# Kernel optimization log

Hardware: AMD Instinct MI355X
Metric: run time of the kernel (lower is better)

## Reference

```python
import jax, jax.numpy as jnp
import numpy as np

N, E, D, H = 50000, 640000, 128, 8
d = D // H  # per-head dim


def layernorm(x, g, b, eps=1e-5):
    mu = jnp.mean(x, axis=-1, keepdims=True)
    var = jnp.var(x, axis=-1, keepdims=True)
    return (x - mu) * jax.lax.rsqrt(var + eps) * g + b


def setup_inputs() -> dict:
    key = jax.random.key(0)
    ks = jax.random.split(key, 14)
    s = 0.05
    return {
        "node_emb": jax.random.normal(ks[0], (N, D), jnp.float32),
        "bond_emb": jax.random.normal(ks[1], (E, D), jnp.float32),
        "basic_attn": jax.random.uniform(ks[2], (E,), jnp.float32),
        "src": jax.random.randint(ks[3], (E,), 0, N),
        "dst": jax.random.randint(ks[4], (E,), 0, N),
        "Wk": jax.random.normal(ks[5], (D, D), jnp.float32) * s,
        "Wq": jax.random.normal(ks[6], (D, D), jnp.float32) * s,
        "Wv": jax.random.normal(ks[7], (D, D), jnp.float32) * s,
        "W_dis": jax.random.normal(ks[8], (1, H), jnp.float32) * s,
        "W_beta": jax.random.normal(ks[9], (3 * D, 1), jnp.float32) * s,
        "ln1_g": jnp.ones((D,), jnp.float32),
        "ln1_b": jnp.zeros((D,), jnp.float32),
        "W_ff1": jax.random.normal(ks[10], (D, 2 * D), jnp.float32) * s,
        "W_ff2": jax.random.normal(ks[11], (2 * D, D), jnp.float32) * s,
    }


def reference(node_emb, bond_emb, basic_attn, src, dst, Wk, Wq, Wv, W_dis,
              W_beta, ln1_g, ln1_b, W_ff1, W_ff2):
    n = node_emb.shape[0]
    # Q/K/V projections (eval mode: dropouts are identity)
    k = (node_emb @ Wk).reshape(n, H, d)
    q = (node_emb @ Wq).reshape(n, H, d)
    v = (bond_emb @ Wv).reshape(-1, H, d)          # per-edge values [E,H,d]
    # per-edge dot-product score (fn.u_dot_v) scaled by sqrt(out_feat)
    scores = jnp.einsum('ehd,ehd->eh', k[src], q[dst])
    scores = scores / jnp.sqrt(jnp.asarray(d, scores.dtype))
    # learned distance decay: Linear(1,H) on basic_attn
    dist = basic_attn[:, None] @ W_dis             # [E,H]
    logits = scores + dist
    # edge_softmax over in-edges of each destination node, per head
    mx = jax.ops.segment_max(logits, dst, num_segments=n)
    mx = jnp.where(jnp.isfinite(mx), mx, 0.0)
    e = jnp.exp(logits - mx[dst])
    den = jax.ops.segment_sum(e, dst, num_segments=n)
    att = e / (den[dst] + 1e-16)                   # [E,H]
    # message = v * att, scatter-sum to destination nodes
    ft = jax.ops.segment_sum(v * att[:, :, None], dst, num_segments=n)
    he = ft.reshape(n, D)
    # beta gating
    beta = jax.nn.sigmoid(
        jnp.concatenate([he, node_emb, he - node_emb], axis=-1) @ W_beta)
    he = beta * node_emb + (1.0 - beta) * he
    # FFN with pre-LN and identity-initialized post-LN
    h = layernorm(he, ln1_g, ln1_b)
    out = jax.nn.relu(h @ W_ff1) @ W_ff2
    ones = jnp.ones((D,), he.dtype)
    zeros = jnp.zeros((D,), he.dtype)
    return layernorm(out + he, ones, zeros)
```

## Files before the change

### kernel.cpp

```cpp
#include <hip/hip_runtime.h>
#include <math.h>

#define NN 50000
#define NE 640000
#define DIM 128
#define NH 8

typedef unsigned short u16;
typedef __attribute__((ext_vector_type(8))) short short8;
typedef __attribute__((ext_vector_type(4))) float f32x4;

__device__ __forceinline__ float wave_sum64(float v) {
  #pragma unroll
  for (int m = 32; m >= 1; m >>= 1) v += __shfl_xor(v, m, 64);
  return v;
}
__device__ __forceinline__ unsigned bf16pk(float a, float b) {
  unsigned ua = __float_as_uint(a); ua = (ua + 0x7fffu + ((ua >> 16) & 1u)) >> 16;
  unsigned ub = __float_as_uint(b); ub = (ub + 0x7fffu + ((ub >> 16) & 1u)) & 0xffff0000u;
  return ua | ub;
}
__device__ __forceinline__ u16 bf16c(float x) {
  unsigned u = __float_as_uint(x);
  return (u16)((u + 0x7fffu + ((u >> 16) & 1u)) >> 16);
}
__device__ __forceinline__ float bf_lo(unsigned v) { return __uint_as_float(v << 16); }
__device__ __forceinline__ float bf_hi(unsigned v) { return __uint_as_float(v & 0xffff0000u); }

#define AS1(p) ((const __attribute__((address_space(1))) unsigned*)(p))
#define AS3(p) ((__attribute__((address_space(3))) unsigned*)(p))

__global__ __launch_bounds__(256) void prep_k(
    const float* __restrict__ node, unsigned* __restrict__ node16,
    const float* __restrict__ Wq, const float* __restrict__ Wk,
    const float* __restrict__ W1, const float* __restrict__ W2,
    u16* __restrict__ Wtq, u16* __restrict__ Wtk,
    u16* __restrict__ Wt1, u16* __restrict__ Wt2,
    const int* __restrict__ dst, int* __restrict__ deg) {
  int b = blockIdx.x, tid = threadIdx.x;
  if (b < 12500) {
    int t = b * 256 + tid;
    float2 v = *(const float2*)(node + (size_t)2 * t);
    node16[t] = bf16pk(v.x, v.y);
  } else if (b < 12564) {
    int t = (b - 12500) * 256 + tid;
    int n = t >> 7, k = t & 127;
    Wtq[t] = bf16c(Wq[(size_t)k * 128 + n]);
  } else if (b < 12628) {
    int t = (b - 12564) * 256 + tid;
    int n = t >> 7, k = t & 127;
    Wtk[t] = bf16c(Wk[(size_t)k * 128 + n]);
  } else if (b < 12756) {
    int t = (b - 12628) * 256 + tid;
    int n = t >> 7, k = t & 127;
    Wt1[t] = bf16c(W1[(size_t)k * 256 + n]);
  } else if (b < 12884) {
    int t = (b - 12756) * 256 + tid;
    int n = t >> 8, k = t & 255;
    Wt2[t] = bf16c(W2[(size_t)k * 128 + n]);
  } else {
    int e = (b - 12884) * 256 + tid;
    atomicAdd(&deg[dst[e]], 1);
  }
}

#define SCAN_T 1024
#define SCHUNK 49
__global__ __launch_bounds__(1024) void scan_k(const int* __restrict__ deg,
                                               int* __restrict__ off,
                                               int* __restrict__ cursor) {
  __shared__ int part[SCAN_T];
  int t = threadIdx.x;
  int lo = t * SCHUNK, hi = lo + SCHUNK; if (hi > NN) hi = NN;
  int s = 0;
  for (int i = lo; i < hi; ++i) s += deg[i];
  part[t] = s;
  __syncthreads();
  for (int o = 1; o < SCAN_T; o <<= 1) {
    int v = (t >= o) ? part[t - o] : 0;
    __syncthreads();
    part[t] += v;
    __syncthreads();
  }
  int base = (t == 0) ? 0 : part[t - 1];
  for (int i = lo; i < hi; ++i) {
    off[i] = base; cursor[i] = base; base += deg[i];
  }
  if (t == SCAN_T - 1) off[NN] = part[SCAN_T - 1];
}

__global__ __launch_bounds__(256) void csr_fill_k(const int* __restrict__ dst,
                                                  int* __restrict__ cursor,
                                                  int* __restrict__ eids) {
  int e = blockIdx.x * 256 + threadIdx.x;
  if (e < NE) {
    int p = atomicAdd(&cursor[dst[e]], 1);
    eids[p] = e;
  }
}

__global__ __launch_bounds__(256) void qk_mfma_k(
    const u16* __restrict__ A, const u16* __restrict__ Wtq,
    const u16* __restrict__ Wtk, u16* __restrict__ qo,
    u16* __restrict__ ko) {
  __shared__ u16 At[64 * 128];
  const int wid = threadIdx.x >> 6, l = threadIdx.x & 63;
  const int quad = l >> 4, l16 = l & 15;
  const int c0 = (wid & 1) * 64;
  const u16* wt = (wid < 2) ? Wtq : Wtk;
  u16* ob = (wid < 2) ? qo : ko;
  short8 bfr[4][4];
  #pragma unroll
  for (int ct = 0; ct < 4; ++ct)
    #pragma unroll
    for (int ks = 0; ks < 4; ++ks)
      bfr[ct][ks] = *(const short8*)(wt + (c0 + ct * 16 + l16) * 128 + ks * 32 + quad * 8);
  const int ntiles = (NN + 63) / 64;
  for (int t = blockIdx.x; t < ntiles; t += gridDim.x) {
    const char* gsrc = (const char*)A + (size_t)t * 64 * 128 * 2;
    #pragma unroll
    for (int i = 0; i < 4; ++i) {
      int dbase = wid * 4096 + i * 1024;
      int soff = (dbase + l * 16) ^ ((((i * 4) + (l >> 4)) & 7) << 4);
      __builtin_amdgcn_global_load_lds(AS1(gsrc + soff),
                                       AS3((char*)At + dbase), 16, 0, 0);
    }
    __syncthreads();
    f32x4 acc[4][4];
    #pragma unroll
    for (int rt = 0; rt < 4; ++rt)
      #pragma unroll
      for (int ct = 0; ct < 4; ++ct)
        acc[rt][ct] = (f32x4){0.f, 0.f, 0.f, 0.f};
    #pragma unroll
    for (int ks = 0; ks < 4; ++ks) {
      short8 af[4];
      #pragma unroll
      for (int rt = 0; rt < 4; ++rt) {
        int bo = (((rt * 16 + l16) * 128 + ks * 32 + quad * 8) * 2) ^ ((l16 & 7) << 4);
        af[rt] = *(const short8*)((const char*)At + bo);
      }
      #pragma unroll
      for (int rt = 0; rt < 4; ++rt)
        #pragma unroll
        for (int ct = 0; ct < 4; ++ct)
          acc[rt][ct] = __builtin_amdgcn_mfma_f32_16x16x32_bf16(
              af[rt], bfr[ct][ks], acc[rt][ct], 0, 0, 0);
    }
    __syncthreads();
    #pragma unroll
    for (int rt = 0; rt < 4; ++rt)
      #pragma unroll
      for (int r = 0; r < 4; ++r) {
        int row = t * 64 + rt * 16 + quad * 4 + r;
        if (row < NN) {
          u16* op = ob + (size_t)row * 128 + c0 + l16;
          #pragma unroll
          for (int ct = 0; ct < 4; ++ct) op[ct * 16] = bf16c(acc[rt][ct][r]);
        }
      }
  }
}

__global__ __launch_bounds__(256) void ffn_mfma_k(
    const u16* __restrict__ A, const u16* __restrict__ Wt1,
    const u16* __restrict__ Wt2, const float* __restrict__ he,
    float* __restrict__ outp) {
  __shared__ __align__(16) u16 At[64 * 128];
  __shared__ __align__(16) u16 Ht[64 * 256];
  __shared__ float redS[4][64], redQ[4][64];
  const int wid = threadIdx.x >> 6, l = threadIdx.x & 63;
  const int quad = l >> 4, l16 = l & 15;
  const int c1 = wid * 64;
  const int c2 = wid * 32;
  const int ntiles = (NN + 63) / 64;
  for (int t = blockIdx.x; t < ntiles; t += gridDim.x) {
    short8 b1f[4][4];
    #pragma unroll
    for (int ct = 0; ct < 4; ++ct)
      #pragma unroll
      for (int ks = 0; ks < 4; ++ks)
        b1f[ct][ks] = *(const short8*)(Wt1 + (c1 + ct * 16 + l16) * 128 + ks * 32 + quad * 8);
    const char* gsrc = (const char*)A + (size_t)t * 64 * 128 * 2;
    #pragma unroll
    for (int i = 0; i < 4; ++i) {
      int dbase = wid * 4096 + i * 1024;
      int soff = (dbase + l * 16) ^ ((((i * 4) + (l >> 4)) & 7) << 4);
      __builtin_amdgcn_global_load_lds(AS1(gsrc + soff),
                                       AS3((char*)At + dbase), 16, 0, 0);
    }
    __syncthreads();
    f32x4 acc1[4][4];
    #pragma unroll
    for (int rt = 0; rt < 4; ++rt)
      #pragma unroll
      for (int ct = 0; ct < 4; ++ct)
        acc1[rt][ct] = (f32x4){0.f, 0.f, 0.f, 0.f};
    #pragma unroll
    for (int ks = 0; ks < 4; ++ks) {
      short8 af[4];
      #pragma unroll
      for (int rt = 0; rt < 4; ++rt) {
        int bo = (((rt * 16 + l16) * 128 + ks * 32 + quad * 8) * 2) ^ ((l16 & 7) << 4);
        af[rt] = *(const short8*)((const char*)At + bo);
      }
      #pragma unroll
      for (int rt = 0; rt < 4; ++rt)
        #pragma unroll
        for (int ct = 0; ct < 4; ++ct)
          acc1[rt][ct] = __builtin_amdgcn_mfma_f32_16x16x32_bf16(
              af[rt], b1f[ct][ks], acc1[rt][ct], 0, 0, 0);
    }
    #pragma unroll
    for (int rt = 0; rt < 4; ++rt)
      #pragma unroll
      for (int r = 0; r < 4; ++r) {
        int row = rt * 16 + quad * 4 + r;
        #pragma unroll
        for (int ct = 0; ct < 4; ++ct) {
          int col = c1 + ct * 16 + l16;
          int bo = (row * 512 + col * 2) ^ ((row & 7) << 4);
          *(u16*)((char*)Ht + bo) = bf16c(fmaxf(acc1[rt][ct][r], 0.f));
        }
      }
    __syncthreads();
    short8 b2f[2][8];
    #pragma unroll
    for (int ct = 0; ct < 2; ++ct)
      #pragma unroll
      for (int ks = 0; ks < 8; ++ks)
        b2f[ct][ks] = *(const short8*)(Wt2 + (c2 + ct * 16 + l16) * 256 + ks * 32 + quad * 8);
    f32x4 acc2[4][2];
    #pragma unroll
    for (int rt = 0; rt < 4; ++rt)
      #pragma unroll
      for (int ct = 0; ct < 2; ++ct)
        acc2[rt][ct] = (f32x4){0.f, 0.f, 0.f, 0.f};
    #pragma unroll
    for (int ks = 0; ks < 8; ++ks) {
      short8 af[4];
      #pragma unroll
      for (int rt = 0; rt < 4; ++rt) {
        int bo = ((rt * 16 + l16) * 512 + ks * 64 + quad * 16) ^ ((l16 & 7) << 4);
        af[rt] = *(const short8*)((const char*)Ht + bo);
      }
      #pragma unroll
      for (int rt = 0; rt < 4; ++rt)
        #pragma unroll
        for (int ct = 0; ct < 2; ++ct)
          acc2[rt][ct] = __builtin_amdgcn_mfma_f32_16x16x32_bf16(
              af[rt], b2f[ct][ks], acc2[rt][ct], 0, 0, 0);
    }
    #pragma unroll
    for (int rt = 0; rt < 4; ++rt)
      #pragma unroll
      for (int r = 0; r < 4; ++r) {
        int row = rt * 16 + quad * 4 + r;
        int grow = t * 64 + row;
        float h0 = 0.f, h1 = 0.f;
        if (grow < NN) {
          h0 = he[(size_t)grow * 128 + c2 + l16];
          h1 = he[(size_t)grow * 128 + c2 + 16 + l16];
        }
        float z0 = acc2[rt][0][r] + h0;
        float z1 = acc2[rt][1][r] + h1;
        acc2[rt][0][r] = z0; acc2[rt][1][r] = z1;
        float ps = z0 + z1;
        float pq = fmaf(z0, z0, z1 * z1);
        ps += __shfl_xor(ps, 1, 64);  pq += __shfl_xor(pq, 1, 64);
        ps += __shfl_xor(ps, 2, 64);  pq += __shfl_xor(pq, 2, 64);
        ps += __shfl_xor(ps, 4, 64);  pq += __shfl_xor(pq, 4, 64);
        ps += __shfl_xor(ps, 8, 64);  pq += __shfl_xor(pq, 8, 64);
        if (l16 == 0) { redS[wid][row] = ps; redQ[wid][row] = pq; }
      }
    __syncthreads();
    #pragma unroll
    for (int rt = 0; rt < 4; ++rt)
      #pragma unroll
      for (int r = 0; r < 4; ++r) {
        int row = rt * 16 + quad * 4 + r;
        int grow = t * 64 + row;
        float s4 = redS[0][row] + redS[1][row] + redS[2][row] + redS[3][row];
        float q4 = redQ[0][row] + redQ[1][row] + redQ[2][row] + redQ[3][row];
        float mu = s4 * (1.f / 128.f);
        float vr = q4 * (1.f / 128.f) - mu * mu;
        float rs = rsqrtf(vr + 1e-5f);
        if (grow < NN) {
          outp[(size_t)grow * 128 + c2 + l16]      = (acc2[rt][0][r] - mu) * rs;
          outp[(size_t)grow * 128 + c2 + 16 + l16] = (acc2[rt][1][r] - mu) * rs;
        }
      }
  }
}

__global__ __launch_bounds__(256) void edge_exp_k(
    const unsigned* __restrict__ kb16, const unsigned* __restrict__ qb16,
    const float* __restrict__ ba, const int* __restrict__ src,
    const int* __restrict__ dst, const float* __restrict__ Wdis,
    const int* __restrict__ eids, float* __restrict__ exs) {
  int idx = blockIdx.x * 256 + threadIdx.x;
  if (idx >= NE * NH) return;
  int p = idx >> 3, h = idx & 7;
  int e = eids[p];
  int s = src[e], t = dst[e];
  const uint4* kp = (const uint4*)(kb16 + (size_t)s * 64 + h * 8);
  const uint4* qp = (const uint4*)(qb16 + (size_t)t * 64 + h * 8);
  uint4 A0 = kp[0], A1 = kp[1];
  uint4 B0 = qp[0], B1 = qp[1];
  float sc = 0.f;
  sc = fmaf(bf_lo(A0.x), bf_lo(B0.x), sc); sc = fmaf(bf_hi(A0.x), bf_hi(B0.x), sc);
  sc = fmaf(bf_lo(A0.y), bf_lo(B0.y), sc); sc = fmaf(bf_hi(A0.y), bf_hi(B0.y), sc);
  sc = fmaf(bf_lo(A0.z), bf_lo(B0.z), sc); sc = fmaf(bf_hi(A0.z), bf_hi(B0.z), sc);
  sc = fmaf(bf_lo(A0.w), bf_lo(B0.w), sc); sc = fmaf(bf_hi(A0.w), bf_hi(B0.w), sc);
  sc = fmaf(bf_lo(A1.x), bf_lo(B1.x), sc); sc = fmaf(bf_hi(A1.x), bf_hi(B1.x), sc);
  sc = fmaf(bf_lo(A1.y), bf_lo(B1.y), sc); sc = fmaf(bf_hi(A1.y), bf_hi(B1.y), sc);
  sc = fmaf(bf_lo(A1.z), bf_lo(B1.z), sc); sc = fmaf(bf_hi(A1.z), bf_hi(B1.z), sc);
  sc = fmaf(bf_lo(A1.w), bf_lo(B1.w), sc); sc = fmaf(bf_hi(A1.w), bf_hi(B1.w), sc);
  exs[idx] = __expf(sc * 0.25f + ba[e] * Wdis[h]);
}

__global__ __launch_bounds__(512, 6) void node_attn_k(
    const float* __restrict__ bond, const float* __restrict__ WvG,
    const float* __restrict__ exs, const int* __restrict__ off,
    const int* __restrict__ eids, const float* __restrict__ x,
    const float* __restrict__ Wb, const float* __restrict__ g1,
    const float* __restrict__ b1, float* __restrict__ he,
    unsigned* __restrict__ hbuf16) {
  __shared__ unsigned Wvpk[DIM * 64];
  __shared__ unsigned gbuf[8][NH][67];
  for (int t = threadIdx.x; t < DIM * 64; t += 512) {
    int i = t >> 6, c = t & 63;
    Wvpk[t] = bf16pk(WvG[i * DIM + c], WvG[i * DIM + c + 64]);
  }
  __syncthreads();
  const int wid = threadIdx.x >> 6, l = threadIdx.x & 63;
  const int hh = l & 7;
  const float wb0 = Wb[l],         wb1 = Wb[l + 64];
  const float wb2 = Wb[DIM + l],   wb3 = Wb[DIM + l + 64];
  const float wb4 = Wb[2*DIM + l], wb5 = Wb[2*DIM + l + 64];
  const float gl0 = g1[l], gl1 = g1[l + 64];
  const float bl0 = b1[l], bl1 = b1[l + 64];

  for (int n = blockIdx.x * 8 + wid; n < NN; n += gridDim.x * 8) {
    int o0 = __builtin_amdgcn_readfirstlane(off[n]);
    int o1 = __builtin_amdgcn_readfirstlane(off[n + 1]);
    int deg = o1 - o0;
    float acc[16];
    #pragma unroll
    for (int i = 0; i < 16; ++i) acc[i] = 0.f;
    float d0 = 0.f, d1 = 0.f, d2 = 0.f, d3 = 0.f;
    float d4 = 0.f, d5 = 0.f, d6 = 0.f, d7 = 0.f;

    for (int g = 0; g < deg; g += 8) {
      float2 bc[8];
      #pragma unroll
      for (int s = 0; s < 8; ++s) {
        if (g + s < deg) {
          int e = eids[o0 + g + s];
          bc[s] = *(const float2*)(bond + (size_t)e * DIM + 2 * l);
        }
      }
      #pragma unroll
      for (int s = 0; s < 8; ++s) {
        if (g + s < deg) {
          const float4* ep = (const float4*)(exs) + (size_t)(o0 + g + s) * 2;
          float4 ea = ep[0], eb = ep[1];
          d0 += ea.x; d1 += ea.y; d2 += ea.z; d3 += ea.w;
          d4 += eb.x; d5 += eb.y; d6 += eb.z; d7 += eb.w;
          float2 bv = bc[s];
          acc[0]  = fmaf(ea.x, bv.x, acc[0]);  acc[1]  = fmaf(ea.x, bv.y, acc[1]);
          acc[2]  = fmaf(ea.y, bv.x, acc[2]);  acc[3]  = fmaf(ea.y, bv.y, acc[3]);
          acc[4]  = fmaf(ea.z, bv.x, acc[4]);  acc[5]  = fmaf(ea.z, bv.y, acc[5]);
          acc[6]  = fmaf(ea.w, bv.x, acc[6]);  acc[7]  = fmaf(ea.w, bv.y, acc[7]);
          acc[8]  = fmaf(eb.x, bv.x, acc[8]);  acc[9]  = fmaf(eb.x, bv.y, acc[9]);
          acc[10] = fmaf(eb.y, bv.x, acc[10]); acc[11] = fmaf(eb.y, bv.y, acc[11]);
          acc[12] = fmaf(eb.z, bv.x, acc[12]); acc[13] = fmaf(eb.z, bv.y, acc[13]);
          acc[14] = fmaf(eb.w, bv.x, acc[14]); acc[15] = fmaf(eb.w, bv.y, acc[15]);
        }
      }
    }
    float dsa = (hh & 1) ? d1 : d0, dsb = (hh & 1) ? d3 : d2;
    float dsc = (hh & 1) ? d5 : d4, dsd = (hh & 1) ? d7 : d6;
    float dse = (hh & 2) ? dsb : dsa, dsf = (hh & 2) ? dsd : dsc;
    float dsel = (hh & 4) ? dsf : dse;
    float rden = 1.f / (dsel + 1e-16f);
    #pragma unroll
    for (int h = 0; h < 8; ++h) {
      float rh = __shfl(rden, h, 64);
      acc[2 * h] *= rh; acc[2 * h + 1] *= rh;
    }
    #pragma unroll
    for (int h = 0; h < 8; ++h)
      gbuf[wid][h][l] = bf16pk(acc[2 * h], acc[2 * h + 1]);
    int h0 = l >> 4, h1 = 4 + (l >> 4);
    float f0 = 0.f, f1 = 0.f;
    #pragma unroll 8
    for (int ii = 0; ii < 64; ++ii) {
      unsigned u = gbuf[wid][h0][ii];
      unsigned v = gbuf[wid][h1][ii];
      unsigned w0 = Wvpk[(2 * ii) * 64 + l];
      unsigned w1 = Wvpk[(2 * ii + 1) * 64 + l];
      f0 = fmaf(bf_lo(u), bf_lo(w0), f0); f0 = fmaf(bf_hi(u), bf_lo(w1), f0);
      f1 = fmaf(bf_lo(v), bf_hi(w0), f1); f1 = fmaf(bf_hi(v), bf_hi(w1), f1);
    }
    float x0 = x[(size_t)n * DIM + l], x1 = x[(size_t)n * DIM + l + 64];
    float s = f0 * wb0 + x0 * wb2 + (f0 - x0) * wb4
            + f1 * wb1 + x1 * wb3 + (f1 - x1) * wb5;
    s = wave_sum64(s);
    float beta = 1.f / (1.f + __expf(-s));
    float he0 = beta * x0 + (1.f - beta) * f0;
    float he1 = beta * x1 + (1.f - beta) * f1;
    he[(size_t)n * DIM + l] = he0;
    he[(size_t)n * DIM + l + 64] = he1;
    float mu = wave_sum64(he0 + he1) * (1.f / DIM);
    float vr = wave_sum64(he0 * he0 + he1 * he1) * (1.f / DIM) - mu * mu;
    float rs = rsqrtf(vr + 1e-5f);
    float v0 = (he0 - mu) * rs * gl0 + bl0;
    float v1 = (he1 - mu) * rs * gl1 + bl1;
    int i0 = (2 * l) & 63, i1 = (2 * l + 1) & 63;
    float a0 = __shfl(v0, i0, 64), b0 = __shfl(v1, i0, 64);
    float a1 = __shfl(v0, i1, 64), b1v = __shfl(v1, i1, 64);
    float c0 = (l < 32) ? a0 : b0;
    float c1 = (l < 32) ? a1 : b1v;
    hbuf16[(size_t)n * 64 + l] = bf16pk(c0, c1);
  }
}

extern "C" void kernel_launch(void* const* d_in, const int* in_sizes, int n_in,
                              void* d_out, int out_size, void* d_ws, size_t ws_size,
                              hipStream_t stream) {
  const float* node = (const float*)d_in[0];
  const float* bond = (const float*)d_in[1];
  const float* ba   = (const float*)d_in[2];
  const int*   src  = (const int*)  d_in[3];
  const int*   dst  = (const int*)  d_in[4];
  const float* Wk   = (const float*)d_in[5];
  const float* Wq   = (const float*)d_in[6];
  const float* Wv   = (const float*)d_in[7];
  const float* Wdis = (const float*)d_in[8];
  const float* Wb   = (const float*)d_in[9];
  const float* g1   = (const float*)d_in[10];
  const float* b1   = (const float*)d_in[11];
  const float* W1   = (const float*)d_in[12];
  const float* W2   = (const float*)d_in[13];
  float* out = (float*)d_out;

  char* W = (char*)d_ws;
  u16* node16 = (u16*)(W);
  u16* qb16   = (u16*)(W + 13000000);
  u16* kb16   = (u16*)(W + 26000000);
  u16* hbuf16 = (u16*)(W + 26000000);
  float* exs  = (float*)(W + 39000000);
  float* he   = (float*)(W + 64600000);
  u16* Wtq    = (u16*)(W + 90200000);
  u16* Wtk    = Wtq + 128 * 128;
  u16* Wt1    = Wtk + 128 * 128;
  u16* Wt2    = Wt1 + 256 * 128;
  int* deg    = (int*)(W + 90400000);
  int* off    = deg + (NN + 1);
  int* cursor = off + (NN + 1);
  int* eids   = cursor + (NN + 1);

  hipMemsetAsync(deg, 0, (size_t)(NN + 1) * 4, stream);

  prep_k<<<15384, 256, 0, stream>>>(node, (unsigned*)node16, Wq, Wk, W1, W2,
                                    Wtq, Wtk, Wt1, Wt2, dst, deg);
  scan_k<<<1, 1024, 0, stream>>>(deg, off, cursor);
  csr_fill_k<<<(NE + 255) / 256, 256, 0, stream>>>(dst, cursor, eids);

  const int ntiles = (NN + 63) / 64;

  qk_mfma_k<<<ntiles, 256, 0, stream>>>(node16, Wtq, Wtk, qb16, kb16);

  edge_exp_k<<<(NE * NH + 255) / 256, 256, 0, stream>>>(
      (const unsigned*)kb16, (const unsigned*)qb16, ba, src, dst, Wdis, eids, exs);

  node_attn_k<<<3125, 512, 0, stream>>>(bond, Wv, exs, off, eids, node,
                                        Wb, g1, b1, he, (unsigned*)hbuf16);

  ffn_mfma_k<<<ntiles, 256, 0, stream>>>(hbuf16, Wt1, Wt2, he, out);
}
```

Before: 858.6 us.

## Fuse edge score and exp computation into node attention kernel

Removes the separate edge_exp_k kernel and computes the per-edge q·k dot product, distance bias and exp inside node_attn_k. Each lane loads one packed bf16 pair of k for the source node, reduces over the 8 lanes of a head with xor shuffles, and broadcasts the per-head exp values across the wave. This drops the exs buffer write and read and one kernel launch, in exchange for extra shuffles and a dependent src gather inside the aggregation loop. The gbuf row is also padded to 68 words and read as 16-byte vectors in the Wv projection loop.

```diff
diff --git a/kernel.cpp b/kernel.cpp
--- a/kernel.cpp
+++ b/kernel.cpp
@@ -293,48 +293,24 @@
   }
 }
 
-__global__ __launch_bounds__(256) void edge_exp_k(
-    const unsigned* __restrict__ kb16, const unsigned* __restrict__ qb16,
-    const float* __restrict__ ba, const int* __restrict__ src,
-    const int* __restrict__ dst, const float* __restrict__ Wdis,
-    const int* __restrict__ eids, float* __restrict__ exs) {
-  int idx = blockIdx.x * 256 + threadIdx.x;
-  if (idx >= NE * NH) return;
-  int p = idx >> 3, h = idx & 7;
-  int e = eids[p];
-  int s = src[e], t = dst[e];
-  const uint4* kp = (const uint4*)(kb16 + (size_t)s * 64 + h * 8);
-  const uint4* qp = (const uint4*)(qb16 + (size_t)t * 64 + h * 8);
-  uint4 A0 = kp[0], A1 = kp[1];
-  uint4 B0 = qp[0], B1 = qp[1];
-  float sc = 0.f;
-  sc = fmaf(bf_lo(A0.x), bf_lo(B0.x), sc); sc = fmaf(bf_hi(A0.x), bf_hi(B0.x), sc);
-  sc = fmaf(bf_lo(A0.y), bf_lo(B0.y), sc); sc = fmaf(bf_hi(A0.y), bf_hi(B0.y), sc);
-  sc = fmaf(bf_lo(A0.z), bf_lo(B0.z), sc); sc = fmaf(bf_hi(A0.z), bf_hi(B0.z), sc);
-  sc = fmaf(bf_lo(A0.w), bf_lo(B0.w), sc); sc = fmaf(bf_hi(A0.w), bf_hi(B0.w), sc);
-  sc = fmaf(bf_lo(A1.x), bf_lo(B1.x), sc); sc = fmaf(bf_hi(A1.x), bf_hi(B1.x), sc);
-  sc = fmaf(bf_lo(A1.y), bf_lo(B1.y), sc); sc = fmaf(bf_hi(A1.y), bf_hi(B1.y), sc);
-  sc = fmaf(bf_lo(A1.z), bf_lo(B1.z), sc); sc = fmaf(bf_hi(A1.z), bf_hi(B1.z), sc);
-  sc = fmaf(bf_lo(A1.w), bf_lo(B1.w), sc); sc = fmaf(bf_hi(A1.w), bf_hi(B1.w), sc);
-  exs[idx] = __expf(sc * 0.25f + ba[e] * Wdis[h]);
-}
-
 __global__ __launch_bounds__(512, 6) void node_attn_k(
     const float* __restrict__ bond, const float* __restrict__ WvG,
-    const float* __restrict__ exs, const int* __restrict__ off,
-    const int* __restrict__ eids, const float* __restrict__ x,
+    const unsigned* __restrict__ qb16, const unsigned* __restrict__ kb16,
+    const float* __restrict__ ba, const int* __restrict__ srcv,
+    const int* __restrict__ off, const int* __restrict__ eids,
+    const float* __restrict__ x, const float* __restrict__ Wdis,
     const float* __restrict__ Wb, const float* __restrict__ g1,
     const float* __restrict__ b1, float* __restrict__ he,
     unsigned* __restrict__ hbuf16) {
   __shared__ unsigned Wvpk[DIM * 64];
-  __shared__ unsigned gbuf[8][NH][67];
+  __shared__ __align__(16) unsigned gbuf[8][NH][68];
   for (int t = threadIdx.x; t < DIM * 64; t += 512) {
     int i = t >> 6, c = t & 63;
     Wvpk[t] = bf16pk(WvG[i * DIM + c], WvG[i * DIM + c + 64]);
   }
   __syncthreads();
   const int wid = threadIdx.x >> 6, l = threadIdx.x & 63;
-  const int hh = l & 7;
+  const float wdis_l = Wdis[l >> 3];
   const float wb0 = Wb[l],         wb1 = Wb[l + 64];
   const float wb2 = Wb[DIM + l],   wb3 = Wb[DIM + l + 64];
   const float wb4 = Wb[2*DIM + l], wb5 = Wb[2*DIM + l + 64];
@@ -345,63 +321,76 @@
     int o0 = __builtin_amdgcn_readfirstlane(off[n]);
     int o1 = __builtin_amdgcn_readfirstlane(off[n + 1]);
     int deg = o1 - o0;
+    unsigned ql = qb16[(size_t)n * 64 + l];
+    float qlo = bf_lo(ql), qhi = bf_hi(ql);
     float acc[16];
     #pragma unroll
     for (int i = 0; i < 16; ++i) acc[i] = 0.f;
-    float d0 = 0.f, d1 = 0.f, d2 = 0.f, d3 = 0.f;
-    float d4 = 0.f, d5 = 0.f, d6 = 0.f, d7 = 0.f;
+    float dsum = 0.f;
 
     for (int g = 0; g < deg; g += 8) {
-      float2 bc[8];
+      int eg[8]; unsigned kc[8]; float2 bc[8];
       #pragma unroll
       for (int s = 0; s < 8; ++s) {
         if (g + s < deg) {
           int e = eids[o0 + g + s];
+          eg[s] = e;
+          kc[s] = kb16[(size_t)srcv[e] * 64 + l];
           bc[s] = *(const float2*)(bond + (size_t)e * DIM + 2 * l);
         }
       }
       #pragma unroll
       for (int s = 0; s < 8; ++s) {
         if (g + s < deg) {
-          const float4* ep = (const float4*)(exs) + (size_t)(o0 + g + s) * 2;
-          float4 ea = ep[0], eb = ep[1];
-          d0 += ea.x; d1 += ea.y; d2 += ea.z; d3 += ea.w;
-          d4 += eb.x; d5 += eb.y; d6 += eb.z; d7 += eb.w;
+          float p = bf_lo(kc[s]) * qlo;
+          p = fmaf(bf_hi(kc[s]), qhi, p);
+          p += __shfl_xor(p, 1, 64);
+          p += __shfl_xor(p, 2, 64);
+          p += __shfl_xor(p, 4, 64);
+          float ex = __expf(fmaf(ba[eg[s]], wdis_l, p * 0.25f));
+          dsum += ex;
+          float a0 = __shfl(ex, 0, 64),  a1 = __shfl(ex, 8, 64);
+          float a2 = __shfl(ex, 16, 64), a3 = __shfl(ex, 24, 64);
+          float a4 = __shfl(ex, 32, 64), a5 = __shfl(ex, 40, 64);
+          float a6 = __shfl(ex, 48, 64), a7 = __shfl(ex, 56, 64);
           float2 bv = bc[s];
-          acc[0]  = fmaf(ea.x, bv.x, acc[0]);  acc[1]  = fmaf(ea.x, bv.y, acc[1]);
-          acc[2]  = fmaf(ea.y, bv.x, acc[2]);  acc[3]  = fmaf(ea.y, bv.y, acc[3]);
-          acc[4]  = fmaf(ea.z, bv.x, acc[4]);  acc[5]  = fmaf(ea.z, bv.y, acc[5]);
-          acc[6]  = fmaf(ea.w, bv.x, acc[6]);  acc[7]  = fmaf(ea.w, bv.y, acc[7]);
-          acc[8]  = fmaf(eb.x, bv.x, acc[8]);  acc[9]  = fmaf(eb.x, bv.y, acc[9]);
-          acc[10] = fmaf(eb.y, bv.x, acc[10]); acc[11] = fmaf(eb.y, bv.y, acc[11]);
-          acc[12] = fmaf(eb.z, bv.x, acc[12]); acc[13] = fmaf(eb.z, bv.y, acc[13]);
-          acc[14] = fmaf(eb.w, bv.x, acc[14]); acc[15] = fmaf(eb.w, bv.y, acc[15]);
-        }
-      }
-    }
-    float dsa = (hh & 1) ? d1 : d0, dsb = (hh & 1) ? d3 : d2;
-    float dsc = (hh & 1) ? d5 : d4, dsd = (hh & 1) ? d7 : d6;
-    float dse = (hh & 2) ? dsb : dsa, dsf = (hh & 2) ? dsd : dsc;
-    float dsel = (hh & 4) ? dsf : dse;
-    float rden = 1.f / (dsel + 1e-16f);
+          acc[0]  = fmaf(a0, bv.x, acc[0]);  acc[1]  = fmaf(a0, bv.y, acc[1]);
+          acc[2]  = fmaf(a1, bv.x, acc[2]);  acc[3]  = fmaf(a1, bv.y, acc[3]);
+          acc[4]  = fmaf(a2, bv.x, acc[4]);  acc[5]  = fmaf(a2, bv.y, acc[5]);
+          acc[6]  = fmaf(a3, bv.x, acc[6]);  acc[7]  = fmaf(a3, bv.y, acc[7]);
+          acc[8]  = fmaf(a4, bv.x, acc[8]);  acc[9]  = fmaf(a4, bv.y, acc[9]);
+          acc[10] = fmaf(a5, bv.x, acc[10]); acc[11] = fmaf(a5, bv.y, acc[11]);
+          acc[12] = fmaf(a6, bv.x, acc[12]); acc[13] = fmaf(a6, bv.y, acc[13]);
+          acc[14] = fmaf(a7, bv.x, acc[14]); acc[15] = fmaf(a7, bv.y, acc[15]);
+        }
+      }
+    }
+    float rden = 1.f / (dsum + 1e-16f);
     #pragma unroll
     for (int h = 0; h < 8; ++h) {
-      float rh = __shfl(rden, h, 64);
+      float rh = __shfl(rden, 8 * h, 64);
       acc[2 * h] *= rh; acc[2 * h + 1] *= rh;
     }
     #pragma unroll
     for (int h = 0; h < 8; ++h)
       gbuf[wid][h][l] = bf16pk(acc[2 * h], acc[2 * h + 1]);
     int h0 = l >> 4, h1 = 4 + (l >> 4);
+    const uint4* gu = (const uint4*)(&gbuf[wid][h0][0]);
+    const uint4* gv = (const uint4*)(&gbuf[wid][h1][0]);
     float f0 = 0.f, f1 = 0.f;
-    #pragma unroll 8
-    for (int ii = 0; ii < 64; ++ii) {
-      unsigned u = gbuf[wid][h0][ii];
-      unsigned v = gbuf[wid][h1][ii];
-      unsigned w0 = Wvpk[(2 * ii) * 64 + l];
-      unsigned w1 = Wvpk[(2 * ii + 1) * 64 + l];
-      f0 = fmaf(bf_lo(u), bf_lo(w0), f0); f0 = fmaf(bf_hi(u), bf_lo(w1), f0);
-      f1 = fmaf(bf_lo(v), bf_hi(w0), f1); f1 = fmaf(bf_hi(v), bf_hi(w1), f1);
+    #pragma unroll
+    for (int q4 = 0; q4 < 16; ++q4) {
+      uint4 U = gu[q4], V = gv[q4];
+      #pragma unroll
+      for (int j = 0; j < 4; ++j) {
+        unsigned u = (j == 0) ? U.x : (j == 1) ? U.y : (j == 2) ? U.z : U.w;
+        unsigned v = (j == 0) ? V.x : (j == 1) ? V.y : (j == 2) ? V.z : V.w;
+        int ii = q4 * 4 + j;
+        unsigned w0 = Wvpk[(2 * ii) * 64 + l];
+        unsigned w1 = Wvpk[(2 * ii + 1) * 64 + l];
+        f0 = fmaf(bf_lo(u), bf_lo(w0), f0); f0 = fmaf(bf_hi(u), bf_lo(w1), f0);
+        f1 = fmaf(bf_lo(v), bf_hi(w0), f1); f1 = fmaf(bf_hi(v), bf_hi(w1), f1);
+      }
     }
     float x0 = x[(size_t)n * DIM + l], x1 = x[(size_t)n * DIM + l + 64];
     float s = f0 * wb0 + x0 * wb2 + (f0 - x0) * wb4
@@ -449,8 +438,7 @@
   u16* node16 = (u16*)(W);
   u16* qb16   = (u16*)(W + 13000000);
   u16* kb16   = (u16*)(W + 26000000);
-  u16* hbuf16 = (u16*)(W + 26000000);
-  float* exs  = (float*)(W + 39000000);
+  u16* hbuf16 = (u16*)(W + 39000000);
   float* he   = (float*)(W + 64600000);
   u16* Wtq    = (u16*)(W + 90200000);
   u16* Wtk    = Wtq + 128 * 128;
@@ -472,11 +460,10 @@
 
   qk_mfma_k<<<ntiles, 256, 0, stream>>>(node16, Wtq, Wtk, qb16, kb16);
 
-  edge_exp_k<<<(NE * NH + 255) / 256, 256, 0, stream>>>(
-      (const unsigned*)kb16, (const unsigned*)qb16, ba, src, dst, Wdis, eids, exs);
-
-  node_attn_k<<<3125, 512, 0, stream>>>(bond, Wv, exs, off, eids, node,
-                                        Wb, g1, b1, he, (unsigned*)hbuf16);
+  node_attn_k<<<3125, 512, 0, stream>>>(bond, Wv, (const unsigned*)qb16,
+                                        (const unsigned*)kb16, ba, src, off,
+                                        eids, node, Wdis, Wb, g1, b1, he,
+                                        (unsigned*)hbuf16);
 
   ffn_mfma_k<<<ntiles, 256, 0, stream>>>(hbuf16, Wt1, Wt2, he, out);
 }
```

After: 1.933 ms. 2.25x slower.

## Rewrite degree scan as coalesced wave-shuffle rounds and deepen bond gather batching

Applied to the files above, without the earlier changes.

The single-block scan switches from per-thread serial chunks to 49 rounds of coalesced 1024-element loads. Each round does a wave shuffle scan followed by a cross-wave scan with a running base, which removes strided uncoalesced reads and the long shared-memory Hillis-Steele loop. Separately, node_attn_k now gathers 16 bond rows per batch instead of 8 to keep more memory loads in flight. To pay for the extra registers, its occupancy hint drops from 6 to 4 waves per SIMD, which may hide latency less well.

```diff
diff --git a/kernel.cpp b/kernel.cpp
--- a/kernel.cpp
+++ b/kernel.cpp
@@ -64,29 +64,45 @@
   }
 }
 
-#define SCAN_T 1024
-#define SCHUNK 49
+#define NROUND 49
 __global__ __launch_bounds__(1024) void scan_k(const int* __restrict__ deg,
                                                int* __restrict__ off,
                                                int* __restrict__ cursor) {
-  __shared__ int part[SCAN_T];
+  __shared__ int wsum[16];
+  __shared__ int roundbase;
   int t = threadIdx.x;
-  int lo = t * SCHUNK, hi = lo + SCHUNK; if (hi > NN) hi = NN;
-  int s = 0;
-  for (int i = lo; i < hi; ++i) s += deg[i];
-  part[t] = s;
+  int lane = t & 63, w = t >> 6;
+  if (t == 0) roundbase = 0;
   __syncthreads();
-  for (int o = 1; o < SCAN_T; o <<= 1) {
-    int v = (t >= o) ? part[t - o] : 0;
-    __syncthreads();
-    part[t] += v;
-    __syncthreads();
-  }
-  int base = (t == 0) ? 0 : part[t - 1];
-  for (int i = lo; i < hi; ++i) {
-    off[i] = base; cursor[i] = base; base += deg[i];
-  }
-  if (t == SCAN_T - 1) off[NN] = part[SCAN_T - 1];
+  for (int r = 0; r < NROUND; ++r) {
+    int i = r * 1024 + t;
+    int v = (i < NN) ? deg[i] : 0;
+    int s = v;
+    #pragma unroll
+    for (int m = 1; m < 64; m <<= 1) {
+      int u = __shfl_up(s, m, 64);
+      if (lane >= m) s += u;
+    }
+    if (lane == 63) wsum[w] = s;
+    __syncthreads();
+    if (w == 0) {
+      int ws = (lane < 16) ? wsum[lane] : 0;
+      #pragma unroll
+      for (int m = 1; m < 16; m <<= 1) {
+        int u = __shfl_up(ws, m, 64);
+        if (lane >= m) ws += u;
+      }
+      if (lane < 16) wsum[lane] = ws;
+    }
+    __syncthreads();
+    int base = roundbase + ((w > 0) ? wsum[w - 1] : 0);
+    int excl = base + s - v;
+    if (i < NN) { off[i] = excl; cursor[i] = excl; }
+    __syncthreads();
+    if (t == 0) roundbase += wsum[15];
+    __syncthreads();
+  }
+  if (t == 0) off[NN] = roundbase;
 }
 
 __global__ __launch_bounds__(256) void csr_fill_k(const int* __restrict__ dst,
@@ -319,7 +335,7 @@
   exs[idx] = __expf(sc * 0.25f + ba[e] * Wdis[h]);
 }
 
-__global__ __launch_bounds__(512, 6) void node_attn_k(
+__global__ __launch_bounds__(512, 4) void node_attn_k(
     const float* __restrict__ bond, const float* __restrict__ WvG,
     const float* __restrict__ exs, const int* __restrict__ off,
     const int* __restrict__ eids, const float* __restrict__ x,
@@ -351,17 +367,17 @@
     float d0 = 0.f, d1 = 0.f, d2 = 0.f, d3 = 0.f;
     float d4 = 0.f, d5 = 0.f, d6 = 0.f, d7 = 0.f;
 
-    for (int g = 0; g < deg; g += 8) {
-      float2 bc[8];
-      #pragma unroll
-      for (int s = 0; s < 8; ++s) {
+    for (int g = 0; g < deg; g += 16) {
+      float2 bc[16];
+      #pragma unroll
+      for (int s = 0; s < 16; ++s) {
         if (g + s < deg) {
           int e = eids[o0 + g + s];
           bc[s] = *(const float2*)(bond + (size_t)e * DIM + 2 * l);
         }
       }
       #pragma unroll
-      for (int s = 0; s < 8; ++s) {
+      for (int s = 0; s < 16; ++s) {
         if (g + s < deg) {
           const float4* ep = (const float4*)(exs) + (size_t)(o0 + g + s) * 2;
           float4 ea = ep[0], eb = ep[1];
```

Result: faster. 830.5 us (-3.3%).
